# Kernel tuning notes

Measured on AMD Instinct MI355X. Metric: run time of the kernel, lower is better.

Reference implementation:

```python
import jax, jax.numpy as jnp
import numpy as np

GROUPS = 32
EPS = 1e-5

def group_norm(x, w, b):
    # x: [B, C, T]
    B, C, T = x.shape
    g = x.reshape(B, GROUPS, C // GROUPS, T)
    mu = g.mean(axis=(2, 3), keepdims=True)
    var = g.var(axis=(2, 3), keepdims=True)
    g = (g - mu) * jax.lax.rsqrt(var + EPS)
    return g.reshape(B, C, T) * w[None, :, None] + b[None, :, None]

def conv1x1(x, w, b):
    # x: [B, C, T], w: [O, C], b: [O]
    return jnp.einsum('oc,bct->bot', w, x) + b[None, :, None]

def setup_inputs() -> dict:
    key = jax.random.key(0)
    ks = jax.random.split(key, 10)
    B, C, H, W = 128, 512, 16, 16
    d = {}
    d['criminal_cond'] = jax.random.normal(ks[0], (B, C, H, W), jnp.float32)
    d['morph_cond'] = jax.random.normal(ks[1], (B, C, H, W), jnp.float32)
    d['norm_w'] = jax.random.uniform(ks[2], (C,), jnp.float32, 0.5, 1.5)
    d['norm_b'] = 0.02 * jax.random.normal(ks[3], (C,), jnp.float32)
    d['qkv_w'] = jax.random.normal(ks[4], (3 * C, C), jnp.float32) / np.sqrt(C)
    d['qkv_b'] = 0.02 * jax.random.normal(ks[5], (3 * C,), jnp.float32)
    d['ekv_w'] = jax.random.normal(ks[6], (2 * C, C), jnp.float32) / np.sqrt(C)
    d['ekv_b'] = 0.02 * jax.random.normal(ks[7], (2 * C,), jnp.float32)
    d['proj_w'] = jax.random.normal(ks[8], (C, C), jnp.float32) / np.sqrt(C)
    d['proj_b'] = 0.02 * jax.random.normal(ks[9], (C,), jnp.float32)
    return d

def reference(criminal_cond, morph_cond, norm_w, norm_b, qkv_w, qkv_b, ekv_w, ekv_b, proj_w, proj_b):
    B, C, H, W = criminal_cond.shape
    x = criminal_cond.reshape(B, C, H * W)          # [B, C, T]
    cond = morph_cond.reshape(B, C, H * W)          # [B, C, S], S == T here
    h = group_norm(x, norm_w, norm_b)
    qkv = conv1x1(h, qkv_w, qkv_b)                  # [B, 3C, T]
    q, k, v = jnp.split(qkv, 3, axis=1)
    ekv = conv1x1(cond, ekv_w, ekv_b)               # [B, 2C, S]
    ek, ev = jnp.split(ekv, 2, axis=1)
    k = jnp.concatenate([ek, k], axis=-1)           # [B, C, S+T]
    v = jnp.concatenate([ev, v], axis=-1)
    scale = 1.0 / np.sqrt(np.sqrt(C))               # single head, head_dim = C
    logits = jnp.einsum('bct,bcs->bts', q * scale, k * scale)
    w = jax.nn.softmax(logits, axis=-1)             # [B, T, S+T]
    a = jnp.einsum('bts,bcs->bct', w, v)            # [B, C, T]
    hout = conv1x1(a, proj_w, proj_b)
    attn_out = (x + hout).reshape(B, C, H, W)
    return 2.0 * morph_cond - attn_out
```

## Files before the change

### kernel.cpp

```cpp
#include <hip/hip_runtime.h>
#include <hip/hip_bf16.h>
#include <math.h>

#define NB 128
#define NC 512
#define NT 256
#define NL 512
#define NG 32
#define SCALE2 0.04419417382415922f

typedef __attribute__((ext_vector_type(8))) short bf16x8;
typedef __attribute__((ext_vector_type(4))) float f32x4;
typedef __attribute__((ext_vector_type(4))) unsigned short u16x4;
typedef __hip_bfloat16 bf16;

struct Params {
  const float *x, *morph, *qkvb, *ekvb, *projb;
  const bf16 *wq, *we, *wp;
  bf16 *hT, *mT, *qT, *kfT, *vf, *pr, *aT;
  float *out;
  int b0;
};

enum { M_QKV = 0, M_EKV = 1, M_LOG = 2, M_PV = 3, M_PROJ = 4 };

__device__ inline unsigned short f2bf_bits(float f) {
  bf16 h = __float2bfloat16(f);
  return *reinterpret_cast<unsigned short*>(&h);
}

__device__ inline void gld16(const void* g, void* lds) {
  __builtin_amdgcn_global_load_lds(
      (const __attribute__((address_space(1))) unsigned int*)g,
      (__attribute__((address_space(3))) unsigned int*)lds, 16, 0, 0);
}

__global__ __launch_bounds__(256) void gn_stats_k(const float* __restrict__ x,
                                                  float* __restrict__ stats) {
  const int bg = blockIdx.x;
  const float* p = x + (size_t)bg * 4096;
  float s = 0.f, s2 = 0.f;
  for (int i = threadIdx.x; i < 4096; i += 256) {
    float v = p[i];
    s += v; s2 += v * v;
  }
  for (int off = 32; off; off >>= 1) {
    s  += __shfl_down(s, off);
    s2 += __shfl_down(s2, off);
  }
  __shared__ float red[8];
  const int wave = threadIdx.x >> 6, lane = threadIdx.x & 63;
  if (lane == 0) { red[wave * 2] = s; red[wave * 2 + 1] = s2; }
  __syncthreads();
  if (threadIdx.x == 0) {
    float S = 0.f, S2 = 0.f;
    for (int w = 0; w < 4; ++w) { S += red[w * 2]; S2 += red[w * 2 + 1]; }
    float mu = S * (1.0f / 4096.0f);
    float var = S2 * (1.0f / 4096.0f) - mu * mu;
    stats[bg * 2]     = mu;
    stats[bg * 2 + 1] = rsqrtf(var + 1e-5f);
  }
}

__global__ __launch_bounds__(256) void cvt_k(const float* __restrict__ s,
                                             bf16* __restrict__ d, int n) {
  int i = blockIdx.x * 256 + threadIdx.x;
  if (i < n) d[i] = __float2bfloat16(s[i]);
}

__global__ __launch_bounds__(256) void transpose2_k(const float* __restrict__ x,
                                                    const float* __restrict__ morph,
                                                    bf16* __restrict__ hT,
                                                    bf16* __restrict__ mT,
                                                    const float* __restrict__ stats,
                                                    const float* __restrict__ gnw,
                                                    const float* __restrict__ gnb,
                                                    int b0, int nbc) {
  __shared__ float sm[32][33];
  const int z = blockIdx.z;
  const int norm = (z < nbc) ? 1 : 0;
  const int lb = norm ? z : z - nbc;
  const int gb = b0 + lb;
  const float* src = norm ? x : morph;
  bf16* dst = norm ? hT : mT;
  const int c0 = blockIdx.y * 32, t0 = blockIdx.x * 32;
  const int tx = threadIdx.x & 31, ty = threadIdx.x >> 5;
  const float* s = src + ((size_t)gb * NC + c0) * NT + t0;
  #pragma unroll
  for (int j = 0; j < 4; ++j) {
    int c = ty + j * 8;
    float v = s[c * NT + tx];
    if (norm) {
      int cg = c0 + c;
      float mu = stats[(gb * NG + (cg >> 4)) * 2];
      float rs = stats[(gb * NG + (cg >> 4)) * 2 + 1];
      v = (v - mu) * rs * gnw[cg] + gnb[cg];
    }
    sm[c][tx] = v;
  }
  __syncthreads();
  bf16* d = dst + ((size_t)lb * NT + t0) * NC + c0;
  #pragma unroll
  for (int j = 0; j < 4; ++j)
    d[(size_t)(ty + j * 8) * NC + tx] = __float2bfloat16(sm[tx][ty + j * 8]);
}

template <int MODE>
__global__ __launch_bounds__(256) void gemm_k(Params P) {
  __shared__ unsigned short As[128][32];
  __shared__ unsigned short Bs[128][32];
  const int lb = blockIdx.z, gb = P.b0 + lb;
  const int m0 = blockIdx.y * 128;
  const int n0 = blockIdx.x * 128;
  const int tid = threadIdx.x;
  const int lane = tid & 63, w = tid >> 6;
  const int wr = w >> 1, wc = w & 1;
  const int ln = lane & 15, kq = lane >> 4;

  const bf16 *Ab, *Bb;
  if (MODE == M_QKV)      { Ab = P.hT + (size_t)lb * NT * NC; Bb = P.wq; }
  else if (MODE == M_EKV) { Ab = P.mT + (size_t)lb * NT * NC; Bb = P.we; }
  else if (MODE == M_LOG) { Ab = P.qT + (size_t)lb * NT * NC; Bb = P.kfT + (size_t)lb * NL * NC; }
  else if (MODE == M_PV)  { Ab = P.pr + (size_t)lb * NT * NL; Bb = P.vf + (size_t)lb * NC * NL; }
  else                    { Ab = P.aT + (size_t)lb * NT * NC; Bb = P.wp; }

  const char* Abase = (const char*)(Ab + (size_t)m0 * 512);
  const char* Bbase = (const char*)(Bb + (size_t)n0 * 512);

  const int r_lo = w * 32 + (lane >> 2);
  const int cid16 = (lane & 3) * 16;

  f32x4 acc[4][4] = {};

  for (int k0 = 0; k0 < 512; k0 += 32) {
    const size_t kb = (size_t)k0 * 2 + cid16;
    #pragma unroll
    for (int h = 0; h < 2; ++h) {
      const int rw = r_lo + h * 16;
      gld16(Abase + (size_t)rw * 1024 + kb, (char*)As + w * 2048 + h * 1024);
      gld16(Bbase + (size_t)rw * 1024 + kb, (char*)Bs + w * 2048 + h * 1024);
    }
    __syncthreads();
    bf16x8 af[4], bfr[4];
    #pragma unroll
    for (int i = 0; i < 4; ++i)
      af[i] = *(const bf16x8*)&As[wr * 64 + i * 16 + ln][kq * 8];
    #pragma unroll
    for (int j = 0; j < 4; ++j)
      bfr[j] = *(const bf16x8*)&Bs[wc * 64 + j * 16 + ln][kq * 8];
    #pragma unroll
    for (int i = 0; i < 4; ++i)
      #pragma unroll
      for (int j = 0; j < 4; ++j)
        acc[i][j] = __builtin_amdgcn_mfma_f32_16x16x32_bf16(af[i], bfr[j], acc[i][j], 0, 0, 0);
    __syncthreads();
  }

  #pragma unroll
  for (int i = 0; i < 4; ++i) {
    const int ig = m0 + wr * 64 + i * 16 + kq * 4;
    #pragma unroll
    for (int j = 0; j < 4; ++j) {
      const int jg = n0 + wc * 64 + j * 16 + ln;
      f32x4 a = acc[i][j];
      if (MODE == M_QKV) {
        float bias = P.qkvb[jg];
        if (jg < 512) {
          bf16* d = P.qT + ((size_t)lb * NT + ig) * NC + jg;
          #pragma unroll
          for (int r = 0; r < 4; ++r) d[(size_t)r * NC] = __float2bfloat16(a[r] + bias);
        } else if (jg < 1024) {
          bf16* d = P.kfT + ((size_t)lb * NL + 256 + ig) * NC + (jg - 512);
          #pragma unroll
          for (int r = 0; r < 4; ++r) d[(size_t)r * NC] = __float2bfloat16(a[r] + bias);
        } else {
          u16x4 pk;
          #pragma unroll
          for (int r = 0; r < 4; ++r) pk[r] = f2bf_bits(a[r] + bias);
          *(u16x4*)(P.vf + ((size_t)lb * NC + (jg - 1024)) * NL + 256 + ig) = pk;
        }
      } else if (MODE == M_EKV) {
        float bias = P.ekvb[jg];
        if (jg < 512) {
          bf16* d = P.kfT + ((size_t)lb * NL + ig) * NC + jg;
          #pragma unroll
          for (int r = 0; r < 4; ++r) d[(size_t)r * NC] = __float2bfloat16(a[r] + bias);
        } else {
          u16x4 pk;
          #pragma unroll
          for (int r = 0; r < 4; ++r) pk[r] = f2bf_bits(a[r] + bias);
          *(u16x4*)(P.vf + ((size_t)lb * NC + (jg - 512)) * NL + ig) = pk;
        }
      } else if (MODE == M_LOG) {
        bf16* d = P.pr + ((size_t)lb * NT + ig) * NL + jg;
        #pragma unroll
        for (int r = 0; r < 4; ++r) d[(size_t)r * NL] = __float2bfloat16(a[r] * SCALE2);
      } else if (MODE == M_PV) {
        bf16* d = P.aT + ((size_t)lb * NT + ig) * NC + jg;
        #pragma unroll
        for (int r = 0; r < 4; ++r) d[(size_t)r * NC] = __float2bfloat16(a[r]);
      } else {
        float bias = P.projb[jg];
        const size_t idx = ((size_t)gb * NC + jg) * NT + ig;
        float4 mo = *(const float4*)&P.morph[idx];
        float4 xx = *(const float4*)&P.x[idx];
        f32x4 o;
        o[0] = 2.0f * mo.x - xx.x - (a[0] + bias);
        o[1] = 2.0f * mo.y - xx.y - (a[1] + bias);
        o[2] = 2.0f * mo.z - xx.z - (a[2] + bias);
        o[3] = 2.0f * mo.w - xx.w - (a[3] + bias);
        *(f32x4*)&P.out[idx] = o;
      }
    }
  }
}

__global__ __launch_bounds__(256) void softmax_k(bf16* __restrict__ pr) {
  const size_t row = (size_t)blockIdx.x * 4 + (threadIdx.x >> 6);
  const int lane = threadIdx.x & 63;
  bf16* p = pr + row * NL + lane * 8;
  float v[8];
  float m = -1e30f;
  #pragma unroll
  for (int i = 0; i < 8; ++i) {
    v[i] = __bfloat162float(p[i]);
    m = fmaxf(m, v[i]);
  }
  #pragma unroll
  for (int off = 32; off; off >>= 1) m = fmaxf(m, __shfl_xor(m, off));
  float s = 0.f;
  #pragma unroll
  for (int i = 0; i < 8; ++i) { v[i] = __expf(v[i] - m); s += v[i]; }
  #pragma unroll
  for (int off = 32; off; off >>= 1) s += __shfl_xor(s, off);
  const float inv = 1.0f / s;
  #pragma unroll
  for (int i = 0; i < 8; ++i) p[i] = __float2bfloat16(v[i] * inv);
}

extern "C" void kernel_launch(void* const* d_in, const int* in_sizes, int n_in,
                              void* d_out, int out_size, void* d_ws, size_t ws_size,
                              hipStream_t stream) {
  const float* x     = (const float*)d_in[0];
  const float* morph = (const float*)d_in[1];
  const float* gnw   = (const float*)d_in[2];
  const float* gnb   = (const float*)d_in[3];
  const float* qkvw  = (const float*)d_in[4];
  const float* qkvb  = (const float*)d_in[5];
  const float* ekvw  = (const float*)d_in[6];
  const float* ekvb  = (const float*)d_in[7];
  const float* projw = (const float*)d_in[8];
  const float* projb = (const float*)d_in[9];

  bf16* wq = (bf16*)d_ws;
  bf16* we = wq + 786432;
  bf16* wp = we + 524288;
  float* stats = (float*)(wp + 262144);
  bf16* pb = (bf16*)(stats + 8192);

  const size_t per_b = 917504;
  const size_t fixed = (size_t)(786432 + 524288 + 262144) * 2 + 8192 * 4;
  int nbc = NB;
  while (nbc > 1 && fixed + (size_t)nbc * per_b * 2 > ws_size) nbc >>= 1;

  Params P;
  P.x = x; P.morph = morph; P.qkvb = qkvb; P.ekvb = ekvb; P.projb = projb;
  P.wq = wq; P.we = we; P.wp = wp;
  P.hT  = pb;                         pb += (size_t)nbc * 131072;
  P.mT  = pb;                         pb += (size_t)nbc * 131072;
  P.qT  = pb;                         pb += (size_t)nbc * 131072;
  P.kfT = pb;                         pb += (size_t)nbc * 262144;
  P.vf  = pb;
  P.pr  = P.mT;
  P.aT  = P.hT;
  P.out = (float*)d_out;

  gn_stats_k<<<dim3(NB * NG), dim3(256), 0, stream>>>(x, stats);
  cvt_k<<<dim3(3072), dim3(256), 0, stream>>>(qkvw, wq, 786432);
  cvt_k<<<dim3(2048), dim3(256), 0, stream>>>(ekvw, we, 524288);
  cvt_k<<<dim3(1024), dim3(256), 0, stream>>>(projw, wp, 262144);

  for (int b0 = 0; b0 < NB; b0 += nbc) {
    P.b0 = b0;
    transpose2_k<<<dim3(8, 16, 2 * nbc), dim3(256), 0, stream>>>(
        x, morph, P.hT, P.mT, stats, gnw, gnb, b0, nbc);
    gemm_k<M_QKV> <<<dim3(12, 2, nbc), dim3(256), 0, stream>>>(P);
    gemm_k<M_EKV> <<<dim3(8, 2, nbc),  dim3(256), 0, stream>>>(P);
    gemm_k<M_LOG> <<<dim3(4, 2, nbc),  dim3(256), 0, stream>>>(P);
    softmax_k     <<<dim3(nbc * 64),   dim3(256), 0, stream>>>(P.pr);
    gemm_k<M_PV>  <<<dim3(4, 2, nbc),  dim3(256), 0, stream>>>(P);
    gemm_k<M_PROJ><<<dim3(4, 2, nbc),  dim3(256), 0, stream>>>(P);
  }
}
```

Measured before the change: 583.7 us.

## Fuse logits, softmax, PV and projection into one attention kernel

Replaces the logits GEMM, standalone softmax, PV GEMM and projection GEMM with a single attn_k kernel. Each block handles 32 query rows against all 512 keys and keeps the probabilities and attention output in LDS, so the intermediates no longer round-trip through global memory. The transpose now uses 64x64 tiles with float4 loads and 16-byte stores, gn_stats is vectorised, and the gemm grid is reordered so batch is the fastest dimension. The trade-off is fewer, heavier blocks: 8 per batch with about 60KB LDS each, so occupancy drops and each block re-reads K, V and the projection weights.

```diff
diff --git a/kernel.cpp b/kernel.cpp
--- a/kernel.cpp
+++ b/kernel.cpp
@@ -12,17 +12,18 @@
 typedef __attribute__((ext_vector_type(8))) short bf16x8;
 typedef __attribute__((ext_vector_type(4))) float f32x4;
 typedef __attribute__((ext_vector_type(4))) unsigned short u16x4;
+typedef __attribute__((ext_vector_type(8))) unsigned short u16x8;
 typedef __hip_bfloat16 bf16;
 
 struct Params {
   const float *x, *morph, *qkvb, *ekvb, *projb;
   const bf16 *wq, *we, *wp;
-  bf16 *hT, *mT, *qT, *kfT, *vf, *pr, *aT;
+  bf16 *hT, *mT, *qT, *kfT, *vf;
   float *out;
   int b0;
 };
 
-enum { M_QKV = 0, M_EKV = 1, M_LOG = 2, M_PV = 3, M_PROJ = 4 };
+enum { M_QKV = 0, M_EKV = 1 };
 
 __device__ inline unsigned short f2bf_bits(float f) {
   bf16 h = __float2bfloat16(f);
@@ -38,12 +39,15 @@
 __global__ __launch_bounds__(256) void gn_stats_k(const float* __restrict__ x,
                                                   float* __restrict__ stats) {
   const int bg = blockIdx.x;
-  const float* p = x + (size_t)bg * 4096;
+  const float4* p4 = (const float4*)(x + (size_t)bg * 4096);
   float s = 0.f, s2 = 0.f;
-  for (int i = threadIdx.x; i < 4096; i += 256) {
-    float v = p[i];
-    s += v; s2 += v * v;
-  }
+  #pragma unroll
+  for (int i = 0; i < 4; ++i) {
+    float4 v = p4[threadIdx.x + i * 256];
+    s  += v.x + v.y + v.z + v.w;
+    s2 += v.x * v.x + v.y * v.y + v.z * v.z + v.w * v.w;
+  }
+  #pragma unroll
   for (int off = 32; off; off >>= 1) {
     s  += __shfl_down(s, off);
     s2 += __shfl_down(s2, off);
@@ -76,53 +80,59 @@
                                                     const float* __restrict__ gnw,
                                                     const float* __restrict__ gnb,
                                                     int b0, int nbc) {
-  __shared__ float sm[32][33];
+  __shared__ float sm[64][65];
   const int z = blockIdx.z;
   const int norm = (z < nbc) ? 1 : 0;
   const int lb = norm ? z : z - nbc;
   const int gb = b0 + lb;
   const float* src = norm ? x : morph;
   bf16* dst = norm ? hT : mT;
-  const int c0 = blockIdx.y * 32, t0 = blockIdx.x * 32;
-  const int tx = threadIdx.x & 31, ty = threadIdx.x >> 5;
-  const float* s = src + ((size_t)gb * NC + c0) * NT + t0;
-  #pragma unroll
-  for (int j = 0; j < 4; ++j) {
-    int c = ty + j * 8;
-    float v = s[c * NT + tx];
+  const int t0 = blockIdx.x * 64, c0 = blockIdx.y * 64;
+  const int tx = threadIdx.x & 15, ty = threadIdx.x >> 4;
+  #pragma unroll
+  for (int ci = 0; ci < 4; ++ci) {
+    const int c = ty + ci * 16;
+    const int cg = c0 + c;
+    float4 v = *(const float4*)&src[((size_t)gb * NC + cg) * NT + t0 + tx * 4];
     if (norm) {
-      int cg = c0 + c;
       float mu = stats[(gb * NG + (cg >> 4)) * 2];
       float rs = stats[(gb * NG + (cg >> 4)) * 2 + 1];
-      v = (v - mu) * rs * gnw[cg] + gnb[cg];
-    }
-    sm[c][tx] = v;
-  }
-  __syncthreads();
-  bf16* d = dst + ((size_t)lb * NT + t0) * NC + c0;
-  #pragma unroll
-  for (int j = 0; j < 4; ++j)
-    d[(size_t)(ty + j * 8) * NC + tx] = __float2bfloat16(sm[tx][ty + j * 8]);
+      float wv = gnw[cg], bv = gnb[cg];
+      v.x = (v.x - mu) * rs * wv + bv;
+      v.y = (v.y - mu) * rs * wv + bv;
+      v.z = (v.z - mu) * rs * wv + bv;
+      v.w = (v.w - mu) * rs * wv + bv;
+    }
+    sm[c][tx * 4 + 0] = v.x; sm[c][tx * 4 + 1] = v.y;
+    sm[c][tx * 4 + 2] = v.z; sm[c][tx * 4 + 3] = v.w;
+  }
+  __syncthreads();
+  const int t = threadIdx.x >> 2, cq = threadIdx.x & 3;
+  u16x8 pk0, pk1;
+  #pragma unroll
+  for (int k = 0; k < 8; ++k) pk0[k] = f2bf_bits(sm[cq * 16 + k][t]);
+  #pragma unroll
+  for (int k = 0; k < 8; ++k) pk1[k] = f2bf_bits(sm[cq * 16 + 8 + k][t]);
+  bf16* d = dst + ((size_t)lb * NT + t0 + t) * NC + c0 + cq * 16;
+  *(u16x8*)d = pk0;
+  *(u16x8*)(d + 8) = pk1;
 }
 
 template <int MODE>
 __global__ __launch_bounds__(256) void gemm_k(Params P) {
   __shared__ unsigned short As[128][32];
   __shared__ unsigned short Bs[128][32];
-  const int lb = blockIdx.z, gb = P.b0 + lb;
+  const int lb = blockIdx.x;
   const int m0 = blockIdx.y * 128;
-  const int n0 = blockIdx.x * 128;
+  const int n0 = blockIdx.z * 128;
   const int tid = threadIdx.x;
   const int lane = tid & 63, w = tid >> 6;
   const int wr = w >> 1, wc = w & 1;
   const int ln = lane & 15, kq = lane >> 4;
 
   const bf16 *Ab, *Bb;
-  if (MODE == M_QKV)      { Ab = P.hT + (size_t)lb * NT * NC; Bb = P.wq; }
-  else if (MODE == M_EKV) { Ab = P.mT + (size_t)lb * NT * NC; Bb = P.we; }
-  else if (MODE == M_LOG) { Ab = P.qT + (size_t)lb * NT * NC; Bb = P.kfT + (size_t)lb * NL * NC; }
-  else if (MODE == M_PV)  { Ab = P.pr + (size_t)lb * NT * NL; Bb = P.vf + (size_t)lb * NC * NL; }
-  else                    { Ab = P.aT + (size_t)lb * NT * NC; Bb = P.wp; }
+  if (MODE == M_QKV) { Ab = P.hT + (size_t)lb * NT * NC; Bb = P.wq; }
+  else               { Ab = P.mT + (size_t)lb * NT * NC; Bb = P.we; }
 
   const char* Abase = (const char*)(Ab + (size_t)m0 * 512);
   const char* Bbase = (const char*)(Bb + (size_t)n0 * 512);
@@ -179,7 +189,7 @@
           for (int r = 0; r < 4; ++r) pk[r] = f2bf_bits(a[r] + bias);
           *(u16x4*)(P.vf + ((size_t)lb * NC + (jg - 1024)) * NL + 256 + ig) = pk;
         }
-      } else if (MODE == M_EKV) {
+      } else {
         float bias = P.ekvb[jg];
         if (jg < 512) {
           bf16* d = P.kfT + ((size_t)lb * NL + ig) * NC + jg;
@@ -191,51 +201,194 @@
           for (int r = 0; r < 4; ++r) pk[r] = f2bf_bits(a[r] + bias);
           *(u16x4*)(P.vf + ((size_t)lb * NC + (jg - 512)) * NL + ig) = pk;
         }
-      } else if (MODE == M_LOG) {
-        bf16* d = P.pr + ((size_t)lb * NT + ig) * NL + jg;
-        #pragma unroll
-        for (int r = 0; r < 4; ++r) d[(size_t)r * NL] = __float2bfloat16(a[r] * SCALE2);
-      } else if (MODE == M_PV) {
-        bf16* d = P.aT + ((size_t)lb * NT + ig) * NC + jg;
-        #pragma unroll
-        for (int r = 0; r < 4; ++r) d[(size_t)r * NC] = __float2bfloat16(a[r]);
-      } else {
-        float bias = P.projb[jg];
-        const size_t idx = ((size_t)gb * NC + jg) * NT + ig;
-        float4 mo = *(const float4*)&P.morph[idx];
-        float4 xx = *(const float4*)&P.x[idx];
-        f32x4 o;
-        o[0] = 2.0f * mo.x - xx.x - (a[0] + bias);
-        o[1] = 2.0f * mo.y - xx.y - (a[1] + bias);
-        o[2] = 2.0f * mo.z - xx.z - (a[2] + bias);
-        o[3] = 2.0f * mo.w - xx.w - (a[3] + bias);
-        *(f32x4*)&P.out[idx] = o;
       }
     }
   }
 }
 
-__global__ __launch_bounds__(256) void softmax_k(bf16* __restrict__ pr) {
-  const size_t row = (size_t)blockIdx.x * 4 + (threadIdx.x >> 6);
-  const int lane = threadIdx.x & 63;
-  bf16* p = pr + row * NL + lane * 8;
-  float v[8];
-  float m = -1e30f;
-  #pragma unroll
-  for (int i = 0; i < 8; ++i) {
-    v[i] = __bfloat162float(p[i]);
-    m = fmaxf(m, v[i]);
-  }
-  #pragma unroll
-  for (int off = 32; off; off >>= 1) m = fmaxf(m, __shfl_xor(m, off));
-  float s = 0.f;
-  #pragma unroll
-  for (int i = 0; i < 8; ++i) { v[i] = __expf(v[i] - m); s += v[i]; }
-  #pragma unroll
-  for (int off = 32; off; off >>= 1) s += __shfl_xor(s, off);
-  const float inv = 1.0f / s;
-  #pragma unroll
-  for (int i = 0; i < 8; ++i) p[i] = __float2bfloat16(v[i] * inv);
+__global__ __launch_bounds__(256) void attn_k(Params P) {
+  __shared__ unsigned short Abuf[32][32];
+  __shared__ unsigned short Bbuf[512][32];
+  __shared__ unsigned short Pbuf[32][520];
+  __shared__ float redm[4][32];
+  __shared__ float reds[4][32];
+
+  const int lb = blockIdx.x, gb = P.b0 + lb;
+  const int t0 = blockIdx.y * 32;
+  const int tid = threadIdx.x;
+  const int lane = tid & 63, w = tid >> 6;
+  const int ln = lane & 15, kq = lane >> 4;
+  const int srow = lane >> 2;
+  const int scol = (lane & 3) * 16;
+
+  const char* qg  = (const char*)(P.qT  + ((size_t)lb * NT + t0) * NC);
+  const char* kg  = (const char*)(P.kfT + (size_t)lb * NL * NC);
+  const char* vg  = (const char*)(P.vf  + (size_t)lb * NC * NL);
+  const char* wpg = (const char*)P.wp;
+
+  f32x4 sa[2][8] = {};
+  bf16x8 af[2], bfr[8];
+
+  for (int k0 = 0; k0 < 512; k0 += 32) {
+    const size_t koff = (size_t)k0 * 2 + scol;
+    if (w < 2)
+      gld16(qg + (size_t)(w * 16 + srow) * 1024 + koff, (char*)Abuf + w * 1024);
+    #pragma unroll
+    for (int h = 0; h < 8; ++h)
+      gld16(kg + (size_t)(w * 128 + h * 16 + srow) * 1024 + koff,
+            (char*)Bbuf + w * 8192 + h * 1024);
+    __syncthreads();
+    af[0] = *(const bf16x8*)&Abuf[ln][kq * 8];
+    af[1] = *(const bf16x8*)&Abuf[16 + ln][kq * 8];
+    #pragma unroll
+    for (int j = 0; j < 8; ++j)
+      bfr[j] = *(const bf16x8*)&Bbuf[w * 128 + j * 16 + ln][kq * 8];
+    #pragma unroll
+    for (int i = 0; i < 2; ++i)
+      #pragma unroll
+      for (int j = 0; j < 8; ++j)
+        sa[i][j] = __builtin_amdgcn_mfma_f32_16x16x32_bf16(af[i], bfr[j], sa[i][j], 0, 0, 0);
+    __syncthreads();
+  }
+
+  float mx[2][4], sum[2][4], inv[2][4];
+  #pragma unroll
+  for (int i = 0; i < 2; ++i)
+    #pragma unroll
+    for (int r = 0; r < 4; ++r) {
+      float m = -1e30f;
+      #pragma unroll
+      for (int j = 0; j < 8; ++j) m = fmaxf(m, sa[i][j][r]);
+      mx[i][r] = m;
+    }
+  #pragma unroll
+  for (int off = 1; off < 16; off <<= 1)
+    #pragma unroll
+    for (int i = 0; i < 2; ++i)
+      #pragma unroll
+      for (int r = 0; r < 4; ++r) mx[i][r] = fmaxf(mx[i][r], __shfl_xor(mx[i][r], off));
+  if (ln == 0)
+    #pragma unroll
+    for (int i = 0; i < 2; ++i)
+      #pragma unroll
+      for (int r = 0; r < 4; ++r) redm[w][i * 16 + kq * 4 + r] = mx[i][r];
+  __syncthreads();
+  #pragma unroll
+  for (int i = 0; i < 2; ++i)
+    #pragma unroll
+    for (int r = 0; r < 4; ++r) {
+      const int row = i * 16 + kq * 4 + r;
+      mx[i][r] = fmaxf(fmaxf(redm[0][row], redm[1][row]),
+                       fmaxf(redm[2][row], redm[3][row]));
+      sum[i][r] = 0.f;
+    }
+  #pragma unroll
+  for (int i = 0; i < 2; ++i)
+    #pragma unroll
+    for (int j = 0; j < 8; ++j)
+      #pragma unroll
+      for (int r = 0; r < 4; ++r) {
+        float e = __expf(SCALE2 * (sa[i][j][r] - mx[i][r]));
+        sa[i][j][r] = e;
+        sum[i][r] += e;
+      }
+  #pragma unroll
+  for (int off = 1; off < 16; off <<= 1)
+    #pragma unroll
+    for (int i = 0; i < 2; ++i)
+      #pragma unroll
+      for (int r = 0; r < 4; ++r) sum[i][r] += __shfl_xor(sum[i][r], off);
+  if (ln == 0)
+    #pragma unroll
+    for (int i = 0; i < 2; ++i)
+      #pragma unroll
+      for (int r = 0; r < 4; ++r) reds[w][i * 16 + kq * 4 + r] = sum[i][r];
+  __syncthreads();
+  #pragma unroll
+  for (int i = 0; i < 2; ++i)
+    #pragma unroll
+    for (int r = 0; r < 4; ++r) {
+      const int row = i * 16 + kq * 4 + r;
+      inv[i][r] = 1.0f / (reds[0][row] + reds[1][row] + reds[2][row] + reds[3][row]);
+    }
+  #pragma unroll
+  for (int i = 0; i < 2; ++i)
+    #pragma unroll
+    for (int j = 0; j < 8; ++j)
+      #pragma unroll
+      for (int r = 0; r < 4; ++r)
+        Pbuf[i * 16 + kq * 4 + r][w * 128 + j * 16 + ln] = f2bf_bits(sa[i][j][r] * inv[i][r]);
+  __syncthreads();
+
+  f32x4 oa[2][8] = {};
+  for (int k0 = 0; k0 < 512; k0 += 32) {
+    const size_t koff = (size_t)k0 * 2 + scol;
+    #pragma unroll
+    for (int h = 0; h < 8; ++h)
+      gld16(vg + (size_t)(w * 128 + h * 16 + srow) * 1024 + koff,
+            (char*)Bbuf + w * 8192 + h * 1024);
+    __syncthreads();
+    af[0] = *(const bf16x8*)&Pbuf[ln][k0 + kq * 8];
+    af[1] = *(const bf16x8*)&Pbuf[16 + ln][k0 + kq * 8];
+    #pragma unroll
+    for (int j = 0; j < 8; ++j)
+      bfr[j] = *(const bf16x8*)&Bbuf[w * 128 + j * 16 + ln][kq * 8];
+    #pragma unroll
+    for (int i = 0; i < 2; ++i)
+      #pragma unroll
+      for (int j = 0; j < 8; ++j)
+        oa[i][j] = __builtin_amdgcn_mfma_f32_16x16x32_bf16(af[i], bfr[j], oa[i][j], 0, 0, 0);
+    __syncthreads();
+  }
+
+  #pragma unroll
+  for (int i = 0; i < 2; ++i)
+    #pragma unroll
+    for (int j = 0; j < 8; ++j)
+      #pragma unroll
+      for (int r = 0; r < 4; ++r)
+        Pbuf[i * 16 + kq * 4 + r][w * 128 + j * 16 + ln] = f2bf_bits(oa[i][j][r]);
+  __syncthreads();
+
+  f32x4 za[2][8] = {};
+  for (int k0 = 0; k0 < 512; k0 += 32) {
+    const size_t koff = (size_t)k0 * 2 + scol;
+    #pragma unroll
+    for (int h = 0; h < 8; ++h)
+      gld16(wpg + (size_t)(w * 128 + h * 16 + srow) * 1024 + koff,
+            (char*)Bbuf + w * 8192 + h * 1024);
+    __syncthreads();
+    af[0] = *(const bf16x8*)&Pbuf[ln][k0 + kq * 8];
+    af[1] = *(const bf16x8*)&Pbuf[16 + ln][k0 + kq * 8];
+    #pragma unroll
+    for (int j = 0; j < 8; ++j)
+      bfr[j] = *(const bf16x8*)&Bbuf[w * 128 + j * 16 + ln][kq * 8];
+    #pragma unroll
+    for (int i = 0; i < 2; ++i)
+      #pragma unroll
+      for (int j = 0; j < 8; ++j)
+        za[i][j] = __builtin_amdgcn_mfma_f32_16x16x32_bf16(af[i], bfr[j], za[i][j], 0, 0, 0);
+    __syncthreads();
+  }
+
+  #pragma unroll
+  for (int i = 0; i < 2; ++i) {
+    const int trow = t0 + i * 16 + kq * 4;
+    #pragma unroll
+    for (int j = 0; j < 8; ++j) {
+      const int c = w * 128 + j * 16 + ln;
+      const float bias = P.projb[c];
+      const size_t idx = ((size_t)gb * NC + c) * NT + trow;
+      float4 mo = *(const float4*)&P.morph[idx];
+      float4 xx = *(const float4*)&P.x[idx];
+      f32x4 o;
+      o[0] = 2.0f * mo.x - xx.x - (za[i][j][0] + bias);
+      o[1] = 2.0f * mo.y - xx.y - (za[i][j][1] + bias);
+      o[2] = 2.0f * mo.z - xx.z - (za[i][j][2] + bias);
+      o[3] = 2.0f * mo.w - xx.w - (za[i][j][3] + bias);
+      *(f32x4*)&P.out[idx] = o;
+    }
+  }
 }
 
 extern "C" void kernel_launch(void* const* d_in, const int* in_sizes, int n_in,
@@ -266,13 +419,11 @@
   Params P;
   P.x = x; P.morph = morph; P.qkvb = qkvb; P.ekvb = ekvb; P.projb = projb;
   P.wq = wq; P.we = we; P.wp = wp;
-  P.hT  = pb;                         pb += (size_t)nbc * 131072;
-  P.mT  = pb;                         pb += (size_t)nbc * 131072;
-  P.qT  = pb;                         pb += (size_t)nbc * 131072;
-  P.kfT = pb;                         pb += (size_t)nbc * 262144;
+  P.hT  = pb;  pb += (size_t)nbc * 131072;
+  P.mT  = pb;  pb += (size_t)nbc * 131072;
+  P.qT  = pb;  pb += (size_t)nbc * 131072;
+  P.kfT = pb;  pb += (size_t)nbc * 262144;
   P.vf  = pb;
-  P.pr  = P.mT;
-  P.aT  = P.hT;
   P.out = (float*)d_out;
 
   gn_stats_k<<<dim3(NB * NG), dim3(256), 0, stream>>>(x, stats);
@@ -282,13 +433,10 @@
 
   for (int b0 = 0; b0 < NB; b0 += nbc) {
     P.b0 = b0;
-    transpose2_k<<<dim3(8, 16, 2 * nbc), dim3(256), 0, stream>>>(
+    transpose2_k<<<dim3(4, 8, 2 * nbc), dim3(256), 0, stream>>>(
         x, morph, P.hT, P.mT, stats, gnw, gnb, b0, nbc);
-    gemm_k<M_QKV> <<<dim3(12, 2, nbc), dim3(256), 0, stream>>>(P);
-    gemm_k<M_EKV> <<<dim3(8, 2, nbc),  dim3(256), 0, stream>>>(P);
-    gemm_k<M_LOG> <<<dim3(4, 2, nbc),  dim3(256), 0, stream>>>(P);
-    softmax_k     <<<dim3(nbc * 64),   dim3(256), 0, stream>>>(P.pr);
-    gemm_k<M_PV>  <<<dim3(4, 2, nbc),  dim3(256), 0, stream>>>(P);
-    gemm_k<M_PROJ><<<dim3(4, 2, nbc),  dim3(256), 0, stream>>>(P);
-  }
-}
+    gemm_k<M_QKV><<<dim3(nbc, 2, 12), dim3(256), 0, stream>>>(P);
+    gemm_k<M_EKV><<<dim3(nbc, 2, 8),  dim3(256), 0, stream>>>(P);
+    attn_k       <<<dim3(nbc, 8),     dim3(256), 0, stream>>>(P);
+  }
+}
```

Result: faster. 538.3 us (-7.8%).
